# Performance work log

Hardware: AMD Instinct MI355X
Metric: run time of the kernel (lower is better)

## Reference

```python
import jax, jax.numpy as jnp
import numpy as np

B, T, C, S = 16, 32768, 64, 4  # batch, time, channels, n_sections


def setup_inputs() -> dict:
    key = jax.random.key(0)
    x = jax.random.normal(key, (B, T, C), dtype=jnp.float32)
    # Build STABLE biquad sections (random coeffs would blow up over 32k steps).
    rng = np.random.default_rng(0)
    r = rng.uniform(0.5, 0.9, S)                      # pole radius < 1 -> stable
    th = rng.uniform(0.1, np.pi - 0.1, S)             # pole angle
    a1 = -2.0 * r * np.cos(th)
    a2 = r ** 2
    b = rng.normal(0.0, 0.5, (S, 3))
    sos = np.concatenate([b, np.stack([np.ones(S), a1, a2], axis=1)], axis=1)
    return {"x": x, "sos": jnp.asarray(sos, dtype=jnp.float32)}


def _biquad(sig, b, a):
    # sig: [N, T]; direct-form-I recurrence, exactly the math of lfilter_bg with n_order=3:
    b0, b1, b2 = b[0], b[1], b[2]
    a0, a1, a2 = a[0], a[1], a[2]

    def step(carry, xt):
        x1, x2, y1, y2 = carry
        y = (b0 * xt + b1 * x1 + b2 * x2 - a1 * y1 - a2 * y2) / a0
        return (xt, x1, y, y1), y

    z = jnp.zeros((sig.shape[0],), sig.dtype)
    _, ys = jax.lax.scan(step, (z, z, z, z), sig.T)  # scan over time -> ys [T, N]
    return ys.T


def reference(x, sos):
    # x: [B, T, C] -> transpose(1,2) -> [B, C, T]; lfilter_bg flattens leading dims.
    Bb, Tt, Cc = x.shape
    sig = jnp.transpose(x, (0, 2, 1)).reshape(Bb * Cc, Tt)
    for s in range(sos.shape[0]):  # small fixed cascade of sections
        sig = _biquad(sig, sos[s, :3], sos[s, 3:])
    return jnp.transpose(sig.reshape(Bb, Cc, Tt), (0, 2, 1))
```

## Files before the change

kernel.cpp:

```cpp
#include <hip/hip_runtime.h>


#define TLEN  32768
#define CCH   64
#define BATCH 16
#define NSEC  4
#define CHUNK 128
#define WARM  128
#define SKEW  3

#define NCHUNKS (TLEN / CHUNK)
#define NWAVES  (BATCH * NCHUNKS)
#define BLOCK   256
#define NBLOCKS (NWAVES * 64 / BLOCK)

__global__ __launch_bounds__(BLOCK, 4) void sos_kernel(const float* __restrict__ x,
                                                       const float* __restrict__ sos,
                                                       float* __restrict__ out) {
    const int lane = threadIdx.x & 63;
    const int wid  = blockIdx.x * (BLOCK >> 6) + (threadIdx.x >> 6);
    const int b    = wid >> 8;
    const int k    = wid & (NCHUNKS - 1);
    const int t0   = k * CHUNK;
    const int s0   = (t0 >= WARM) ? (t0 - WARM) : 0;
    const int warm = t0 - s0;

    float cb0[NSEC], cb1[NSEC], cb2[NSEC], ca1[NSEC], ca2[NSEC];
    float x1[NSEC], x2[NSEC], y1v[NSEC], y2v[NSEC];
#pragma unroll
    for (int s = 0; s < NSEC; ++s) {
        const float inva = 1.0f / sos[s * 6 + 3];
        cb0[s] =  sos[s * 6 + 0] * inva;
        cb1[s] =  sos[s * 6 + 1] * inva;
        cb2[s] =  sos[s * 6 + 2] * inva;
        ca1[s] = -sos[s * 6 + 4] * inva;
        ca2[s] = -sos[s * 6 + 5] * inva;
        x1[s] = x2[s] = y1v[s] = y2v[s] = 0.0f;
    }
    float lat1 = 0.0f, lat2 = 0.0f, lat3 = 0.0f;

    const float* __restrict__ xb = x + (size_t)b * TLEN * CCH + lane;
    float* __restrict__ py = out + ((size_t)b * TLEN + (size_t)t0) * CCH + lane;

    const int total  = warm + CHUNK + SKEW;
    const int padded = (total + 7) & ~7;
    const int sfrom  = warm + SKEW;

    float xbuf[8];
#pragma unroll
    for (int j = 0; j < 8; ++j) {
        int idx = s0 + j; if (idx > TLEN - 1) idx = TLEN - 1;
        xbuf[j] = xb[(size_t)idx * CCH];
    }

    for (int g = 0; g < padded; g += 8) {
        float nbuf[8];
#pragma unroll
        for (int j = 0; j < 8; ++j) {
            int idx = s0 + g + 8 + j; if (idx > TLEN - 1) idx = TLEN - 1;
            nbuf[j] = xb[(size_t)idx * CCH];
        }
#pragma unroll
        for (int j = 0; j < 8; ++j) {
            const int i = g + j;
            const float i0 = xbuf[j], i1 = lat1, i2 = lat2, i3 = lat3;
            const float p0 = fmaf(cb0[0], i0, fmaf(cb1[0], x1[0], cb2[0] * x2[0]));
            const float p1 = fmaf(cb0[1], i1, fmaf(cb1[1], x1[1], cb2[1] * x2[1]));
            const float p2 = fmaf(cb0[2], i2, fmaf(cb1[2], x1[2], cb2[2] * x2[2]));
            const float p3 = fmaf(cb0[3], i3, fmaf(cb1[3], x1[3], cb2[3] * x2[3]));
            const float o0 = fmaf(ca1[0], y1v[0], fmaf(ca2[0], y2v[0], p0));
            const float o1 = fmaf(ca1[1], y1v[1], fmaf(ca2[1], y2v[1], p1));
            const float o2 = fmaf(ca1[2], y1v[2], fmaf(ca2[2], y2v[2], p2));
            const float o3 = fmaf(ca1[3], y1v[3], fmaf(ca2[3], y2v[3], p3));
            x2[0] = x1[0]; x1[0] = i0;  y2v[0] = y1v[0]; y1v[0] = o0;
            x2[1] = x1[1]; x1[1] = i1;  y2v[1] = y1v[1]; y1v[1] = o1;
            x2[2] = x1[2]; x1[2] = i2;  y2v[2] = y1v[2]; y1v[2] = o2;
            x2[3] = x1[3]; x1[3] = i3;  y2v[3] = y1v[3]; y1v[3] = o3;
            lat1 = o0; lat2 = o1; lat3 = o2;
            if (i >= sfrom && i < total) {
                py[(size_t)(i - sfrom) * CCH] = o3;
            }
        }
#pragma unroll
        for (int j = 0; j < 8; ++j) xbuf[j] = nbuf[j];
    }
}

extern "C" void kernel_launch(void* const* d_in, const int* in_sizes, int n_in,
                              void* d_out, int out_size, void* d_ws, size_t ws_size,
                              hipStream_t stream) {
    const float* x   = (const float*)d_in[0];
    const float* sos = (const float*)d_in[1];
    float* out = (float*)d_out;
    sos_kernel<<<NBLOCKS, BLOCK, 0, stream>>>(x, sos, out);
}
```

Baseline: 261.3 us.

## Triple-buffer input loads with fixed-trip macro-unrolled groups and shorter warmup

Restructures the time loop into fully unrolled 8-step groups that rotate through three register buffers. Loads for group g+2 are issued while group g computes, which deepens the prefetch distance and removes per-step bounds checks and the buffer copy. The warmup is cut from 128 to 120 steps so the trip counts are compile-time constants (15 warm groups, 16 output groups plus a 3-step tail), and the wave index goes through readfirstlane so it stays scalar. The shorter warmup slightly raises truncation error at chunk boundaries, and the extra buffers raise register pressure.

```diff
diff --git a/kernel.cpp b/kernel.cpp
--- a/kernel.cpp
+++ b/kernel.cpp
@@ -6,7 +6,7 @@
 #define BATCH 16
 #define NSEC  4
 #define CHUNK 128
-#define WARM  128
+#define WARM  120
 #define SKEW  3
 
 #define NCHUNKS (TLEN / CHUNK)
@@ -14,16 +14,61 @@
 #define BLOCK   256
 #define NBLOCKS (NWAVES * 64 / BLOCK)
 
+#define ISSUE(NB, G) do {                                                     \
+    int rb_ = s0 + 8 * (G);                                                   \
+    rb_ = (rb_ > TLEN - 8) ? (TLEN - 8) : rb_;                                \
+    const float* __restrict__ p_ = xb + (size_t)rb_ * CCH;                    \
+    NB[0] = p_[0 * CCH]; NB[1] = p_[1 * CCH];                                 \
+    NB[2] = p_[2 * CCH]; NB[3] = p_[3 * CCH];                                 \
+    NB[4] = p_[4 * CCH]; NB[5] = p_[5 * CCH];                                 \
+    NB[6] = p_[6 * CCH]; NB[7] = p_[7 * CCH];                                 \
+} while (0)
+
+#define STEP(CB, j, ps, SB, SE) do {                                          \
+    const float i0 = CB[j], i1 = lat1, i2 = lat2, i3 = lat3;                  \
+    const float p0 = fmaf(cb0[0], i0, fmaf(cb1[0], x1[0], cb2[0] * x2[0]));   \
+    const float p1 = fmaf(cb0[1], i1, fmaf(cb1[1], x1[1], cb2[1] * x2[1]));   \
+    const float p2 = fmaf(cb0[2], i2, fmaf(cb1[2], x1[2], cb2[2] * x2[2]));   \
+    const float p3 = fmaf(cb0[3], i3, fmaf(cb1[3], x1[3], cb2[3] * x2[3]));   \
+    const float o0 = fmaf(ca1[0], y1v[0], fmaf(ca2[0], y2v[0], p0));          \
+    const float o1 = fmaf(ca1[1], y1v[1], fmaf(ca2[1], y2v[1], p1));          \
+    const float o2 = fmaf(ca1[2], y1v[2], fmaf(ca2[2], y2v[2], p2));          \
+    const float o3 = fmaf(ca1[3], y1v[3], fmaf(ca2[3], y2v[3], p3));          \
+    x2[0] = x1[0]; x1[0] = i0;  y2v[0] = y1v[0]; y1v[0] = o0;                 \
+    x2[1] = x1[1]; x1[1] = i1;  y2v[1] = y1v[1]; y1v[1] = o1;                 \
+    x2[2] = x1[2]; x1[2] = i2;  y2v[2] = y1v[2]; y1v[2] = o2;                 \
+    x2[3] = x1[3]; x1[3] = i3;  y2v[3] = y1v[3]; y1v[3] = o3;                 \
+    lat1 = o0; lat2 = o1; lat3 = o2;                                          \
+    if ((j) >= (SB) && (j) < (SE)) ps[(j) * CCH] = o3;                        \
+} while (0)
+
+#define GROUP(CB, NB, G, H, SB, SE) do {                                      \
+    ISSUE(NB, (G) + 2);                                                       \
+    float* __restrict__ ps = py + (ptrdiff_t)(8 * (H) - 3) * CCH;             \
+    STEP(CB, 0, ps, SB, SE); STEP(CB, 1, ps, SB, SE);                         \
+    STEP(CB, 2, ps, SB, SE); STEP(CB, 3, ps, SB, SE);                         \
+    STEP(CB, 4, ps, SB, SE); STEP(CB, 5, ps, SB, SE);                         \
+    STEP(CB, 6, ps, SB, SE); STEP(CB, 7, ps, SB, SE);                         \
+} while (0)
+
 __global__ __launch_bounds__(BLOCK, 4) void sos_kernel(const float* __restrict__ x,
                                                        const float* __restrict__ sos,
                                                        float* __restrict__ out) {
     const int lane = threadIdx.x & 63;
-    const int wid  = blockIdx.x * (BLOCK >> 6) + (threadIdx.x >> 6);
+    const int wid  = __builtin_amdgcn_readfirstlane(
+                         blockIdx.x * (BLOCK >> 6) + (threadIdx.x >> 6));
     const int b    = wid >> 8;
     const int k    = wid & (NCHUNKS - 1);
     const int t0   = k * CHUNK;
-    const int s0   = (t0 >= WARM) ? (t0 - WARM) : 0;
-    const int warm = t0 - s0;
+    const int warm = k ? WARM : 0;
+    const int s0   = t0 - warm;
+
+    const float* __restrict__ xb = x + (size_t)b * TLEN * CCH + lane;
+    float* __restrict__ py = out + ((size_t)b * TLEN + (size_t)t0) * CCH + lane;
+
+    float Af[8], Bf[8], Cf[8];
+    ISSUE(Af, 0);
+    ISSUE(Bf, 1);
 
     float cb0[NSEC], cb1[NSEC], cb2[NSEC], ca1[NSEC], ca2[NSEC];
     float x1[NSEC], x2[NSEC], y1v[NSEC], y2v[NSEC];
@@ -39,50 +84,29 @@
     }
     float lat1 = 0.0f, lat2 = 0.0f, lat3 = 0.0f;
 
-    const float* __restrict__ xb = x + (size_t)b * TLEN * CCH + lane;
-    float* __restrict__ py = out + ((size_t)b * TLEN + (size_t)t0) * CCH + lane;
-
-    const int total  = warm + CHUNK + SKEW;
-    const int padded = (total + 7) & ~7;
-    const int sfrom  = warm + SKEW;
-
-    float xbuf[8];
-#pragma unroll
-    for (int j = 0; j < 8; ++j) {
-        int idx = s0 + j; if (idx > TLEN - 1) idx = TLEN - 1;
-        xbuf[j] = xb[(size_t)idx * CCH];
+    int g = 0;
+    if (warm) {
+#pragma unroll 1
+        for (int t = 0; t < 5; ++t) {
+            GROUP(Af, Cf, g + 0, 0, 0, 0);
+            GROUP(Bf, Af, g + 1, 0, 0, 0);
+            GROUP(Cf, Bf, g + 2, 0, 0, 0);
+            g += 3;
+        }
     }
-
-    for (int g = 0; g < padded; g += 8) {
-        float nbuf[8];
-#pragma unroll
-        for (int j = 0; j < 8; ++j) {
-            int idx = s0 + g + 8 + j; if (idx > TLEN - 1) idx = TLEN - 1;
-            nbuf[j] = xb[(size_t)idx * CCH];
-        }
-#pragma unroll
-        for (int j = 0; j < 8; ++j) {
-            const int i = g + j;
-            const float i0 = xbuf[j], i1 = lat1, i2 = lat2, i3 = lat3;
-            const float p0 = fmaf(cb0[0], i0, fmaf(cb1[0], x1[0], cb2[0] * x2[0]));
-            const float p1 = fmaf(cb0[1], i1, fmaf(cb1[1], x1[1], cb2[1] * x2[1]));
-            const float p2 = fmaf(cb0[2], i2, fmaf(cb1[2], x1[2], cb2[2] * x2[2]));
-            const float p3 = fmaf(cb0[3], i3, fmaf(cb1[3], x1[3], cb2[3] * x2[3]));
-            const float o0 = fmaf(ca1[0], y1v[0], fmaf(ca2[0], y2v[0], p0));
-            const float o1 = fmaf(ca1[1], y1v[1], fmaf(ca2[1], y2v[1], p1));
-            const float o2 = fmaf(ca1[2], y1v[2], fmaf(ca2[2], y2v[2], p2));
-            const float o3 = fmaf(ca1[3], y1v[3], fmaf(ca2[3], y2v[3], p3));
-            x2[0] = x1[0]; x1[0] = i0;  y2v[0] = y1v[0]; y1v[0] = o0;
-            x2[1] = x1[1]; x1[1] = i1;  y2v[1] = y1v[1]; y1v[1] = o1;
-            x2[2] = x1[2]; x1[2] = i2;  y2v[2] = y1v[2]; y1v[2] = o2;
-            x2[3] = x1[3]; x1[3] = i3;  y2v[3] = y1v[3]; y1v[3] = o3;
-            lat1 = o0; lat2 = o1; lat3 = o2;
-            if (i >= sfrom && i < total) {
-                py[(size_t)(i - sfrom) * CCH] = o3;
-            }
-        }
-#pragma unroll
-        for (int j = 0; j < 8; ++j) xbuf[j] = nbuf[j];
+    GROUP(Af, Cf, g, 0, 3, 8); ++g;
+#pragma unroll 1
+    for (int t = 0; t < 5; ++t) {
+        GROUP(Bf, Af, g + 0, 3 * t + 1, 0, 8);
+        GROUP(Cf, Bf, g + 1, 3 * t + 2, 0, 8);
+        GROUP(Af, Cf, g + 2, 3 * t + 3, 0, 8);
+        g += 3;
+    }
+    {
+        float* __restrict__ ps = py + (ptrdiff_t)(8 * 16 - 3) * CCH;
+        STEP(Bf, 0, ps, 0, 3);
+        STEP(Bf, 1, ps, 0, 3);
+        STEP(Bf, 2, ps, 0, 3);
     }
 }
 
```

After: 251.1 us. 3.9% less time.
